# Kernel optimization log

Hardware: AMD Instinct MI355X
Metric: run time of the kernel (lower is better)

The kernel has to match this reference:

```python
import jax, jax.numpy as jnp
import numpy as np

N_NODES = 100000
N_EDGES = 1600000
IN_DIM = 128
HID_DIM = 64
OUT_DIM = 1


def setup_inputs() -> dict:
    key = jax.random.key(0)
    k = jax.random.split(key, 8)
    x = jax.random.normal(k[0], (N_NODES, IN_DIM), dtype=jnp.float32)
    edge_index = jax.random.randint(k[1], (2, N_EDGES), 0, N_NODES, dtype=jnp.int64)
    # GCNConv layer 1: weight [IN, HID], bias [HID] (glorot-ish scale)
    W1 = jax.random.normal(k[2], (IN_DIM, HID_DIM), dtype=jnp.float32) / np.sqrt(IN_DIM)
    b1 = jnp.zeros((HID_DIM,), dtype=jnp.float32)
    W2 = jax.random.normal(k[3], (HID_DIM, HID_DIM), dtype=jnp.float32) / np.sqrt(HID_DIM)
    b2 = jnp.zeros((HID_DIM,), dtype=jnp.float32)
    Wfc = jax.random.normal(k[4], (HID_DIM, OUT_DIM), dtype=jnp.float32) / np.sqrt(HID_DIM)
    bfc = jnp.zeros((OUT_DIM,), dtype=jnp.float32)
    return {"x": x, "edge_index": edge_index, "W1": W1, "b1": b1,
            "W2": W2, "b2": b2, "Wfc": Wfc, "bfc": bfc}


def _gcn_norm(edge_index, n_nodes):
    # PyG GCNConv default: add self-loops, symmetric normalization.
    src, dst = edge_index[0], edge_index[1]
    loop = jnp.arange(n_nodes, dtype=src.dtype)
    src = jnp.concatenate([src, loop])
    dst = jnp.concatenate([dst, loop])
    deg = jax.ops.segment_sum(jnp.ones_like(dst, dtype=jnp.float32), dst,
                              num_segments=n_nodes)
    deg_isqrt = jax.lax.rsqrt(deg)  # deg >= 1 thanks to self-loops
    norm = deg_isqrt[src] * deg_isqrt[dst]  # [E+N]
    return src, dst, norm


def _gcn_conv(x, src, dst, norm, W, b, n_nodes):
    h = x @ W                      # [N, D_out] dense transform first (D_out <= D_in)
    msg = h[src] * norm[:, None]   # gather + normalize  [E+N, D_out]
    out = jax.ops.segment_sum(msg, dst, num_segments=n_nodes)  # scatter-add
    return out + b


def reference(x, edge_index, W1, b1, W2, b2, Wfc, bfc):
    n = x.shape[0]
    src, dst, norm = _gcn_norm(edge_index, n)
    h = jax.nn.relu(_gcn_conv(x, src, dst, norm, W1, b1, n))
    h = jax.nn.relu(_gcn_conv(h, src, dst, norm, W2, b2, n))
    return h @ Wfc + bfc  # [N, 1]
```

## Files before the change

### kernel.cpp

```cpp
#include <hip/hip_runtime.h>
#include <hip/hip_bf16.h>


#define IN_DIM 128
#define HID 64
#define B1 256
#define MAXNC 512

typedef unsigned int uint;

__device__ inline uint pack_bf16x2(float a, float b) {
    uint ua = __builtin_bit_cast(uint, a);
    uint ub = __builtin_bit_cast(uint, b);
    ua += 0x7fffu + ((ua >> 16) & 1u);
    ub += 0x7fffu + ((ub >> 16) & 1u);
    return (ua >> 16) | (ub & 0xffff0000u);
}
__device__ inline float bf_lo(uint g) { return __builtin_bit_cast(float, g << 16); }
__device__ inline float bf_hi(uint g) { return __builtin_bit_cast(float, g & 0xffff0000u); }

__global__ __launch_bounds__(512) void hist1(const int* __restrict__ dst,
                                             int* __restrict__ ghist,
                                             int E, int NC, int chunk) {
    __shared__ int h[MAXNC];
    int t = threadIdx.x, blk = blockIdx.x;
    if (t < NC) h[t] = 0;
    __syncthreads();
    int s = blk * chunk, e = min(E, s + chunk);
    for (int i = s + t; i < e; i += 512) atomicAdd(&h[dst[i] >> 8], 1);
    __syncthreads();
    if (t < NC) ghist[(size_t)t * B1 + blk] = h[t];
}

__global__ __launch_bounds__(256) void scan_p1(const int* __restrict__ a,
                                               int* __restrict__ bsum, int M) {
    int i = blockIdx.x * 256 + threadIdx.x;
    int v = (i < M) ? a[i] : 0;
#pragma unroll
    for (int o = 32; o; o >>= 1) v += __shfl_down(v, o, 64);
    __shared__ int ws[4];
    int lane = threadIdx.x & 63, wid = threadIdx.x >> 6;
    if (lane == 0) ws[wid] = v;
    __syncthreads();
    if (threadIdx.x == 0) bsum[blockIdx.x] = ws[0] + ws[1] + ws[2] + ws[3];
}

__global__ __launch_bounds__(512) void scan_p2(const int* __restrict__ bsum,
                                               int* __restrict__ boff,
                                               int* __restrict__ row_off,
                                               int nb, int N) {
    __shared__ int s[512];
    int t = threadIdx.x;
    int v = (t < nb) ? bsum[t] : 0;
    s[t] = v;
    __syncthreads();
#pragma unroll
    for (int o = 1; o < 512; o <<= 1) {
        int add = (t >= o) ? s[t - o] : 0;
        __syncthreads();
        s[t] += add;
        __syncthreads();
    }
    if (t < nb) boff[t] = s[t] - v;
    if (t == nb - 1) row_off[N] = s[t];
}

__global__ __launch_bounds__(256) void scan_p3(int* __restrict__ a,
                                               const int* __restrict__ boff, int M) {
    __shared__ int s[256];
    int i = blockIdx.x * 256 + threadIdx.x;
    int t = threadIdx.x;
    int d = (i < M) ? a[i] : 0;
    s[t] = d;
    __syncthreads();
#pragma unroll
    for (int o = 1; o < 256; o <<= 1) {
        int add = (t >= o) ? s[t - o] : 0;
        __syncthreads();
        s[t] += add;
        __syncthreads();
    }
    if (i < M) a[i] = s[t] - d + boff[blockIdx.x];
}

__global__ __launch_bounds__(512) void scatter1(const int* __restrict__ src,
                                                const int* __restrict__ dst,
                                                const int* __restrict__ goff,
                                                uint* __restrict__ pairs,
                                                int E, int NC, int chunk) {
    __shared__ int cur[MAXNC];
    int t = threadIdx.x, blk = blockIdx.x;
    if (t < NC) cur[t] = goff[(size_t)t * B1 + blk];
    __syncthreads();
    int s = blk * chunk, e = min(E, s + chunk);
    for (int i = s + t; i < e; i += 512) {
        int d = dst[i];
        int p = atomicAdd(&cur[d >> 8], 1);
        pairs[p] = ((uint)src[i] << 8) | (uint)(d & 255);
    }
}

__global__ __launch_bounds__(256) void build_csr(const uint* __restrict__ pairs,
                                                 const int* __restrict__ goff,
                                                 int* __restrict__ row_off,
                                                 float* __restrict__ disqrt,
                                                 int* __restrict__ col,
                                                 int E, int NC, int N) {
    __shared__ int h[256], cur[256];
    __shared__ int ws[4], wsoff[4];
    int b = blockIdx.x, t = threadIdx.x;
    int base = goff[(size_t)b * B1];
    int next = (b + 1 < NC) ? goff[(size_t)(b + 1) * B1] : E;
    h[t] = 0;
    __syncthreads();
    for (int i = base + t; i < next; i += 256)
        atomicAdd(&h[pairs[i] & 255u], 1);
    __syncthreads();
    int deg = h[t];
    int incl = deg;
#pragma unroll
    for (int o = 1; o < 64; o <<= 1) {
        int u = __shfl_up(incl, o, 64);
        if ((t & 63) >= o) incl += u;
    }
    if ((t & 63) == 63) ws[t >> 6] = incl;
    __syncthreads();
    if (t == 0) {
        int run = 0;
#pragma unroll
        for (int i = 0; i < 4; ++i) { wsoff[i] = run; run += ws[i]; }
    }
    __syncthreads();
    int excl = wsoff[t >> 6] + incl - deg;
    cur[t] = base + excl;
    int node = (b << 8) + t;
    if (node < N) {
        row_off[node] = base + excl;
        disqrt[node]  = rsqrtf((float)(deg + 1));
    }
    __syncthreads();
    for (int i = base + t; i < next; i += 256) {
        uint p = pairs[i];
        int pos = atomicAdd(&cur[p & 255u], 1);
        col[pos] = (int)(p >> 8);
    }
}

template <int K>
__global__ __launch_bounds__(256) void gemm_tile(const float* __restrict__ X,
                                                 const float* __restrict__ W,
                                                 const float* __restrict__ disqrt,
                                                 uint* __restrict__ Tsb, int n) {
    __shared__ float xs[32][132];
    __shared__ float ws[32][64];
    const int tid = threadIdx.x;
    const int ng  = tid & 15;
    const int mg  = tid >> 4;
    const int m0  = blockIdx.x * 128;
    const float4 z4 = make_float4(0.f, 0.f, 0.f, 0.f);
    int xr[4], xk[4];
#pragma unroll
    for (int i = 0; i < 4; ++i) { int f = tid + i * 256; xr[i] = f >> 3; xk[i] = f & 7; }
    const int wk0 = tid >> 4, wc0 = tid & 15;

    float4 gx[4], gw[2];
#pragma unroll
    for (int i = 0; i < 4; ++i) {
        int row = m0 + xr[i];
        gx[i] = (row < n) ? *(const float4*)(X + (size_t)row * K + 4 * xk[i]) : z4;
    }
    gw[0] = *(const float4*)(W + (size_t)wk0 * 64 + 4 * wc0);
    gw[1] = *(const float4*)(W + (size_t)(wk0 + 16) * 64 + 4 * wc0);

    float acc[8][4] = {};
    for (int kc = 0;;) {
#pragma unroll
        for (int i = 0; i < 4; ++i) {
            xs[4 * xk[i] + 0][xr[i]] = gx[i].x;
            xs[4 * xk[i] + 1][xr[i]] = gx[i].y;
            xs[4 * xk[i] + 2][xr[i]] = gx[i].z;
            xs[4 * xk[i] + 3][xr[i]] = gx[i].w;
        }
        *(float4*)&ws[wk0][4 * wc0]      = gw[0];
        *(float4*)&ws[wk0 + 16][4 * wc0] = gw[1];
        __syncthreads();
        kc += 32;
        const bool more = kc < K;
        if (more) {
#pragma unroll
            for (int i = 0; i < 4; ++i) {
                int row = m0 + xr[i];
                gx[i] = (row < n) ? *(const float4*)(X + (size_t)row * K + kc + 4 * xk[i]) : z4;
            }
            gw[0] = *(const float4*)(W + (size_t)(kc + wk0) * 64 + 4 * wc0);
            gw[1] = *(const float4*)(W + (size_t)(kc + wk0 + 16) * 64 + 4 * wc0);
        }
#pragma unroll 4
        for (int k = 0; k < 32; ++k) {
            float4 a0 = *(const float4*)&xs[k][8 * mg];
            float4 a1 = *(const float4*)&xs[k][8 * mg + 4];
            float4 b  = *(const float4*)&ws[k][4 * ng];
            const float* ap0 = (const float*)&a0;
            const float* ap1 = (const float*)&a1;
            const float* bp  = (const float*)&b;
#pragma unroll
            for (int mi = 0; mi < 4; ++mi)
#pragma unroll
                for (int ni = 0; ni < 4; ++ni) {
                    acc[mi][ni]     += ap0[mi] * bp[ni];
                    acc[mi + 4][ni] += ap1[mi] * bp[ni];
                }
        }
        if (!more) break;
        __syncthreads();
    }
#pragma unroll
    for (int mi = 0; mi < 8; ++mi) {
        int row = m0 + 8 * mg + mi;
        if (row < n) {
            float s = disqrt[row];
            uint2 pk;
            pk.x = pack_bf16x2(acc[mi][0] * s, acc[mi][1] * s);
            pk.y = pack_bf16x2(acc[mi][2] * s, acc[mi][3] * s);
            *(uint2*)(Tsb + (size_t)row * 32 + 2 * ng) = pk;
        }
    }
}

__global__ __launch_bounds__(256) void gemm_tile_b(const uint* __restrict__ Xb,
                                                   const float* __restrict__ W,
                                                   const float* __restrict__ disqrt,
                                                   uint* __restrict__ Tsb, int n) {
    const int K = 64;
    __shared__ float xs[32][132];
    __shared__ float ws[32][64];
    const int tid = threadIdx.x;
    const int ng  = tid & 15;
    const int mg  = tid >> 4;
    const int m0  = blockIdx.x * 128;
    const uint2 z2 = make_uint2(0u, 0u);
    int xr[4], xk[4];
#pragma unroll
    for (int i = 0; i < 4; ++i) { int f = tid + i * 256; xr[i] = f >> 3; xk[i] = f & 7; }
    const int wk0 = tid >> 4, wc0 = tid & 15;

    uint2 gx[4];
    float4 gw[2];
#pragma unroll
    for (int i = 0; i < 4; ++i) {
        int row = m0 + xr[i];
        gx[i] = (row < n) ? *(const uint2*)(Xb + (size_t)row * 32 + 2 * xk[i]) : z2;
    }
    gw[0] = *(const float4*)(W + (size_t)wk0 * 64 + 4 * wc0);
    gw[1] = *(const float4*)(W + (size_t)(wk0 + 16) * 64 + 4 * wc0);

    float acc[8][4] = {};
    for (int kc = 0;;) {
#pragma unroll
        for (int i = 0; i < 4; ++i) {
            xs[4 * xk[i] + 0][xr[i]] = bf_lo(gx[i].x);
            xs[4 * xk[i] + 1][xr[i]] = bf_hi(gx[i].x);
            xs[4 * xk[i] + 2][xr[i]] = bf_lo(gx[i].y);
            xs[4 * xk[i] + 3][xr[i]] = bf_hi(gx[i].y);
        }
        *(float4*)&ws[wk0][4 * wc0]      = gw[0];
        *(float4*)&ws[wk0 + 16][4 * wc0] = gw[1];
        __syncthreads();
        kc += 32;
        const bool more = kc < K;
        if (more) {
#pragma unroll
            for (int i = 0; i < 4; ++i) {
                int row = m0 + xr[i];
                gx[i] = (row < n) ? *(const uint2*)(Xb + (size_t)row * 32 + 16 + 2 * xk[i]) : z2;
            }
            gw[0] = *(const float4*)(W + (size_t)(kc + wk0) * 64 + 4 * wc0);
            gw[1] = *(const float4*)(W + (size_t)(kc + wk0 + 16) * 64 + 4 * wc0);
        }
#pragma unroll 4
        for (int k = 0; k < 32; ++k) {
            float4 a0 = *(const float4*)&xs[k][8 * mg];
            float4 a1 = *(const float4*)&xs[k][8 * mg + 4];
            float4 b  = *(const float4*)&ws[k][4 * ng];
            const float* ap0 = (const float*)&a0;
            const float* ap1 = (const float*)&a1;
            const float* bp  = (const float*)&b;
#pragma unroll
            for (int mi = 0; mi < 4; ++mi)
#pragma unroll
                for (int ni = 0; ni < 4; ++ni) {
                    acc[mi][ni]     += ap0[mi] * bp[ni];
                    acc[mi + 4][ni] += ap1[mi] * bp[ni];
                }
        }
        if (!more) break;
        __syncthreads();
    }
#pragma unroll
    for (int mi = 0; mi < 8; ++mi) {
        int row = m0 + 8 * mg + mi;
        if (row < n) {
            float s = disqrt[row];
            uint2 pk;
            pk.x = pack_bf16x2(acc[mi][0] * s, acc[mi][1] * s);
            pk.y = pack_bf16x2(acc[mi][2] * s, acc[mi][3] * s);
            *(uint2*)(Tsb + (size_t)row * 32 + 2 * ng) = pk;
        }
    }
}

template <bool FUSE_FC>
__global__ __launch_bounds__(256) void agg_kernel(const uint* __restrict__ Tsb,
                                                  const int* __restrict__ row_off,
                                                  const int* __restrict__ col,
                                                  const float* __restrict__ disqrt,
                                                  const float* __restrict__ bias,
                                                  const float* __restrict__ wfc,
                                                  const float* __restrict__ bfc,
                                                  uint* __restrict__ outb,
                                                  float* __restrict__ outf, int n) {
    int node = blockIdx.x * 4 + (threadIdx.x >> 6);
    if (node >= n) return;
    int lane = threadIdx.x & 63;
    int o = lane >> 3;
    int p = lane & 7;
    float acc[8] = {};
    if (o == 0) {
        uint4 g = *(const uint4*)(Tsb + (size_t)node * 32 + 4 * p);
        acc[0] = bf_lo(g.x); acc[1] = bf_hi(g.x);
        acc[2] = bf_lo(g.y); acc[3] = bf_hi(g.y);
        acc[4] = bf_lo(g.z); acc[5] = bf_hi(g.z);
        acc[6] = bf_lo(g.w); acc[7] = bf_hi(g.w);
    }
    int beg = __builtin_amdgcn_readfirstlane(row_off[node]);
    int end = __builtin_amdgcn_readfirstlane(row_off[node + 1]);
    for (int batch = beg; batch < end; batch += 64) {
        int bn = min(64, end - batch);
        int cv = 0;
        if (batch + lane < end) cv = col[batch + lane];
        int j = 0;
        for (; j + 16 <= bn; j += 16) {
            int s0 = __shfl(cv, j + o, 64);
            int s1 = __shfl(cv, j + 8 + o, 64);
            uint4 g0 = *(const uint4*)(Tsb + (size_t)s0 * 32 + 4 * p);
            uint4 g1 = *(const uint4*)(Tsb + (size_t)s1 * 32 + 4 * p);
            acc[0] += bf_lo(g0.x); acc[1] += bf_hi(g0.x);
            acc[2] += bf_lo(g0.y); acc[3] += bf_hi(g0.y);
            acc[4] += bf_lo(g0.z); acc[5] += bf_hi(g0.z);
            acc[6] += bf_lo(g0.w); acc[7] += bf_hi(g0.w);
            acc[0] += bf_lo(g1.x); acc[1] += bf_hi(g1.x);
            acc[2] += bf_lo(g1.y); acc[3] += bf_hi(g1.y);
            acc[4] += bf_lo(g1.z); acc[5] += bf_hi(g1.z);
            acc[6] += bf_lo(g1.w); acc[7] += bf_hi(g1.w);
        }
        for (; j < bn; j += 8) {
            int idx = j + o;
            int s = __shfl(cv, idx & 63, 64);
            uint4 g = *(const uint4*)(Tsb + (size_t)s * 32 + 4 * p);
            if (idx < bn) {
                acc[0] += bf_lo(g.x); acc[1] += bf_hi(g.x);
                acc[2] += bf_lo(g.y); acc[3] += bf_hi(g.y);
                acc[4] += bf_lo(g.z); acc[5] += bf_hi(g.z);
                acc[6] += bf_lo(g.w); acc[7] += bf_hi(g.w);
            }
        }
    }
#pragma unroll
    for (int k = 0; k < 8; ++k) {
        acc[k] += __shfl_xor(acc[k], 8, 64);
        acc[k] += __shfl_xor(acc[k], 16, 64);
        acc[k] += __shfl_xor(acc[k], 32, 64);
    }
    float dq = disqrt[node];
    float4 bv0 = *(const float4*)(bias + 8 * p);
    float4 bv1 = *(const float4*)(bias + 8 * p + 4);
    float r[8];
    r[0] = fmaxf(acc[0] * dq + bv0.x, 0.f);
    r[1] = fmaxf(acc[1] * dq + bv0.y, 0.f);
    r[2] = fmaxf(acc[2] * dq + bv0.z, 0.f);
    r[3] = fmaxf(acc[3] * dq + bv0.w, 0.f);
    r[4] = fmaxf(acc[4] * dq + bv1.x, 0.f);
    r[5] = fmaxf(acc[5] * dq + bv1.y, 0.f);
    r[6] = fmaxf(acc[6] * dq + bv1.z, 0.f);
    r[7] = fmaxf(acc[7] * dq + bv1.w, 0.f);
    if (!FUSE_FC) {
        if (o == 0) {
            uint4 pk;
            pk.x = pack_bf16x2(r[0], r[1]);
            pk.y = pack_bf16x2(r[2], r[3]);
            pk.z = pack_bf16x2(r[4], r[5]);
            pk.w = pack_bf16x2(r[6], r[7]);
            *(uint4*)(outb + (size_t)node * 32 + 4 * p) = pk;
        }
    } else {
        float4 wv0 = *(const float4*)(wfc + 8 * p);
        float4 wv1 = *(const float4*)(wfc + 8 * p + 4);
        float v = r[0] * wv0.x + r[1] * wv0.y + r[2] * wv0.z + r[3] * wv0.w +
                  r[4] * wv1.x + r[5] * wv1.y + r[6] * wv1.z + r[7] * wv1.w;
        v += __shfl_down(v, 4, 64);
        v += __shfl_down(v, 2, 64);
        v += __shfl_down(v, 1, 64);
        if (lane == 0) outf[node] = v + bfc[0];
    }
}

extern "C" void kernel_launch(void* const* d_in, const int* in_sizes, int n_in,
                              void* d_out, int out_size, void* d_ws, size_t ws_size,
                              hipStream_t stream) {
    const float* x   = (const float*)d_in[0];
    const int*   ei  = (const int*)d_in[1];
    const float* W1  = (const float*)d_in[2];
    const float* b1  = (const float*)d_in[3];
    const float* W2  = (const float*)d_in[4];
    const float* b2  = (const float*)d_in[5];
    const float* Wfc = (const float*)d_in[6];
    const float* bfc = (const float*)d_in[7];
    float* out = (float*)d_out;

    const int N = in_sizes[0] / IN_DIM;
    const int E = in_sizes[1] / 2;
    const int* src = ei;
    const int* dst = ei + E;
    const int NC    = (N + 255) >> 8;
    const int chunk = (E + B1 - 1) / B1;
    const int M     = NC * B1;
    const int NBs   = (M + 255) / 256;

    char* w = (char*)d_ws;
    auto alloc = [&](size_t bytes) {
        void* p = (void*)w;
        w += (bytes + 255) & ~(size_t)255;
        return p;
    };
    int*   row_off = (int*)alloc((size_t)(N + 1) * 4);
    float* disqrt  = (float*)alloc((size_t)N * 4);
    int*   goff    = (int*)alloc((size_t)NC * B1 * 4);
    int*   bsum    = (int*)alloc(512 * 4);
    int*   boff    = (int*)alloc(512 * 4);
    int*   col     = (int*)alloc((size_t)E * 4);
    size_t scrA = (size_t)E * 4, scrB = (size_t)N * HID * 2;
    void*  scr  = alloc(scrA > scrB ? scrA : scrB);
    uint*  h1b  = (uint*)alloc((size_t)N * HID * 2);
    uint*  pairs = (uint*)scr;
    uint*  Tsb   = (uint*)scr;

    hist1<<<B1, 512, 0, stream>>>(dst, goff, E, NC, chunk);
    scan_p1<<<NBs, 256, 0, stream>>>(goff, bsum, M);
    scan_p2<<<1, 512, 0, stream>>>(bsum, boff, row_off, NBs, N);
    scan_p3<<<NBs, 256, 0, stream>>>(goff, boff, M);
    scatter1<<<B1, 512, 0, stream>>>(src, dst, goff, pairs, E, NC, chunk);
    build_csr<<<NC, 256, 0, stream>>>(pairs, goff, row_off, disqrt, col, E, NC, N);

    gemm_tile<IN_DIM><<<(N + 127) / 128, 256, 0, stream>>>(x, W1, disqrt, Tsb, N);
    agg_kernel<false><<<(N + 3) / 4, 256, 0, stream>>>(Tsb, row_off, col, disqrt,
                                                       b1, nullptr, nullptr,
                                                       h1b, nullptr, N);

    gemm_tile_b<<<(N + 127) / 128, 256, 0, stream>>>(h1b, W2, disqrt, Tsb, N);
    agg_kernel<true><<<(N + 3) / 4, 256, 0, stream>>>(Tsb, row_off, col, disqrt,
                                                      b2, Wfc, bfc,
                                                      nullptr, out, N);
}
```

Measured before the change: 277.8 us.

## Replace FP32 FMA GEMMs with split-bf16 MFMA matrix-core GEMMs

Replaces the two scalar-FMA tiled GEMM kernels with one templated MFMA kernel using 16x16x32 bf16 instructions. Accuracy is kept by splitting the weights (and the fp32 input of layer 1) into high and low bf16 parts and summing three partial products. The weight split and transpose is folded into the single-block scan_p2 kernel. This adds extra MFMA work and per-element split arithmetic, and the GEMMs were probably a minor share next to the memory-bound aggregation kernels.

```diff
diff --git a/kernel.cpp b/kernel.cpp
--- a/kernel.cpp
+++ b/kernel.cpp
@@ -1,5 +1,4 @@
 #include <hip/hip_runtime.h>
-#include <hip/hip_bf16.h>
 
 
 #define IN_DIM 128
@@ -8,6 +7,9 @@
 #define MAXNC 512
 
 typedef unsigned int uint;
+typedef unsigned short ushort;
+typedef __attribute__((ext_vector_type(8))) short short8;
+typedef __attribute__((ext_vector_type(4))) float f32x4;
 
 __device__ inline uint pack_bf16x2(float a, float b) {
     uint ua = __builtin_bit_cast(uint, a);
@@ -18,6 +20,11 @@
 }
 __device__ inline float bf_lo(uint g) { return __builtin_bit_cast(float, g << 16); }
 __device__ inline float bf_hi(uint g) { return __builtin_bit_cast(float, g & 0xffff0000u); }
+__device__ inline uint rne_hi_bits(float a) {
+    uint u = __builtin_bit_cast(uint, a);
+    return (u + 0x7fffu + ((u >> 16) & 1u)) & 0xffff0000u;
+}
+__device__ inline float bitf(uint u) { return __builtin_bit_cast(float, u); }
 
 __global__ __launch_bounds__(512) void hist1(const int* __restrict__ dst,
                                              int* __restrict__ ghist,
@@ -48,9 +55,36 @@
 __global__ __launch_bounds__(512) void scan_p2(const int* __restrict__ bsum,
                                                int* __restrict__ boff,
                                                int* __restrict__ row_off,
-                                               int nb, int N) {
+                                               int nb, int N,
+                                               const float* __restrict__ W1f,
+                                               const float* __restrict__ W2f,
+                                               ushort* __restrict__ w1h,
+                                               ushort* __restrict__ w1l,
+                                               ushort* __restrict__ w2h,
+                                               ushort* __restrict__ w2l) {
+    int t = threadIdx.x;
+    {
+        int c = t & 63;
+        int kb1 = (t >> 6) * 16;
+#pragma unroll 4
+        for (int kk = 0; kk < 16; ++kk) {
+            int k = kb1 + kk;
+            float v = W1f[k * 64 + c];
+            uint rh = rne_hi_bits(v);
+            w1h[c * 128 + k] = (ushort)(rh >> 16);
+            w1l[c * 128 + k] = (ushort)(rne_hi_bits(v - bitf(rh)) >> 16);
+        }
+        int kb2 = (t >> 6) * 8;
+#pragma unroll 4
+        for (int kk = 0; kk < 8; ++kk) {
+            int k = kb2 + kk;
+            float v = W2f[k * 64 + c];
+            uint rh = rne_hi_bits(v);
+            w2h[c * 64 + k] = (ushort)(rh >> 16);
+            w2l[c * 64 + k] = (ushort)(rne_hi_bits(v - bitf(rh)) >> 16);
+        }
+    }
     __shared__ int s[512];
-    int t = threadIdx.x;
     int v = (t < nb) ? bsum[t] : 0;
     s[t] = v;
     __syncthreads();
@@ -146,165 +180,128 @@
     }
 }
 
-template <int K>
-__global__ __launch_bounds__(256) void gemm_tile(const float* __restrict__ X,
-                                                 const float* __restrict__ W,
+template <int K, bool SPLIT>
+__global__ __launch_bounds__(256) void gemm_mfma(const void* __restrict__ Xv,
+                                                 const ushort* __restrict__ WHt,
+                                                 const ushort* __restrict__ WLt,
                                                  const float* __restrict__ disqrt,
                                                  uint* __restrict__ Tsb, int n) {
-    __shared__ float xs[32][132];
-    __shared__ float ws[32][64];
+    __shared__ ushort XH[128 * 40];
+    __shared__ ushort WH[64 * 40];
+    __shared__ ushort WL[64 * 40];
+    __shared__ ushort XL[SPLIT ? 128 * 40 : 64];
+
     const int tid = threadIdx.x;
-    const int ng  = tid & 15;
-    const int mg  = tid >> 4;
     const int m0  = blockIdx.x * 128;
+    const float* Xf = (const float*)Xv;
+    const char*  Xb = (const char*)Xv;
+
+    const int wc = tid >> 2, wslot = tid & 3;
+    const char* wh_g = (const char*)WHt + wc * (K * 2) + wslot * 16;
+    const char* wl_g = (const char*)WLt + wc * (K * 2) + wslot * 16;
+
+    constexpr int NL = SPLIT ? 4 : 2;
+    int xr[NL], xk[NL];
+#pragma unroll
+    for (int i = 0; i < NL; ++i) {
+        int f = tid + i * 256;
+        if (SPLIT) { xr[i] = f >> 3; xk[i] = f & 7; }
+        else       { xr[i] = f >> 2; xk[i] = f & 3; }
+    }
+
     const float4 z4 = make_float4(0.f, 0.f, 0.f, 0.f);
-    int xr[4], xk[4];
-#pragma unroll
-    for (int i = 0; i < 4; ++i) { int f = tid + i * 256; xr[i] = f >> 3; xk[i] = f & 7; }
-    const int wk0 = tid >> 4, wc0 = tid & 15;
-
-    float4 gx[4], gw[2];
-#pragma unroll
-    for (int i = 0; i < 4; ++i) {
+    const uint4  zu = make_uint4(0u, 0u, 0u, 0u);
+    float4 gx[NL];
+    uint4  gxb[NL];
+    uint4  gwh, gwl;
+#pragma unroll
+    for (int i = 0; i < NL; ++i) {
         int row = m0 + xr[i];
-        gx[i] = (row < n) ? *(const float4*)(X + (size_t)row * K + 4 * xk[i]) : z4;
-    }
-    gw[0] = *(const float4*)(W + (size_t)wk0 * 64 + 4 * wc0);
-    gw[1] = *(const float4*)(W + (size_t)(wk0 + 16) * 64 + 4 * wc0);
-
-    float acc[8][4] = {};
+        if (SPLIT) gx[i]  = (row < n) ? *(const float4*)(Xf + (size_t)row * K + 4 * xk[i]) : z4;
+        else       gxb[i] = (row < n) ? *(const uint4*)(Xb + (size_t)row * (K * 2) + xk[i] * 16) : zu;
+    }
+    gwh = *(const uint4*)wh_g;
+    gwl = *(const uint4*)wl_g;
+
+    f32x4 acc[2][4] = {};
+    const int l   = tid & 63, wv = tid >> 6;
+    const int lr  = l & 15;
+    const int kob = (l >> 4) * 16;
+
     for (int kc = 0;;) {
-#pragma unroll
-        for (int i = 0; i < 4; ++i) {
-            xs[4 * xk[i] + 0][xr[i]] = gx[i].x;
-            xs[4 * xk[i] + 1][xr[i]] = gx[i].y;
-            xs[4 * xk[i] + 2][xr[i]] = gx[i].z;
-            xs[4 * xk[i] + 3][xr[i]] = gx[i].w;
-        }
-        *(float4*)&ws[wk0][4 * wc0]      = gw[0];
-        *(float4*)&ws[wk0 + 16][4 * wc0] = gw[1];
-        __syncthreads();
+        if (SPLIT) {
+#pragma unroll
+            for (int i = 0; i < NL; ++i) {
+                float a = gx[i].x, b = gx[i].y, c = gx[i].z, d = gx[i].w;
+                uint rha = rne_hi_bits(a), rhb = rne_hi_bits(b);
+                uint rhc = rne_hi_bits(c), rhd = rne_hi_bits(d);
+                uint2 hh, ll;
+                hh.x = (rha >> 16) | (rhb & 0xffff0000u);
+                hh.y = (rhc >> 16) | (rhd & 0xffff0000u);
+                ll.x = pack_bf16x2(a - bitf(rha), b - bitf(rhb));
+                ll.y = pack_bf16x2(c - bitf(rhc), d - bitf(rhd));
+                *(uint2*)((char*)XH + xr[i] * 80 + xk[i] * 8) = hh;
+                *(uint2*)((char*)XL + xr[i] * 80 + xk[i] * 8) = ll;
+            }
+        } else {
+#pragma unroll
+            for (int i = 0; i < NL; ++i)
+                *(uint4*)((char*)XH + xr[i] * 80 + xk[i] * 16) = gxb[i];
+        }
+        *(uint4*)((char*)WH + wc * 80 + wslot * 16) = gwh;
+        *(uint4*)((char*)WL + wc * 80 + wslot * 16) = gwl;
+        __syncthreads();
+
         kc += 32;
         const bool more = kc < K;
         if (more) {
 #pragma unroll
-            for (int i = 0; i < 4; ++i) {
+            for (int i = 0; i < NL; ++i) {
                 int row = m0 + xr[i];
-                gx[i] = (row < n) ? *(const float4*)(X + (size_t)row * K + kc + 4 * xk[i]) : z4;
+                if (SPLIT) gx[i]  = (row < n) ? *(const float4*)(Xf + (size_t)row * K + kc + 4 * xk[i]) : z4;
+                else       gxb[i] = (row < n) ? *(const uint4*)(Xb + (size_t)row * (K * 2) + kc * 2 + xk[i] * 16) : zu;
             }
-            gw[0] = *(const float4*)(W + (size_t)(kc + wk0) * 64 + 4 * wc0);
-            gw[1] = *(const float4*)(W + (size_t)(kc + wk0 + 16) * 64 + 4 * wc0);
-        }
-#pragma unroll 4
-        for (int k = 0; k < 32; ++k) {
-            float4 a0 = *(const float4*)&xs[k][8 * mg];
-            float4 a1 = *(const float4*)&xs[k][8 * mg + 4];
-            float4 b  = *(const float4*)&ws[k][4 * ng];
-            const float* ap0 = (const float*)&a0;
-            const float* ap1 = (const float*)&a1;
-            const float* bp  = (const float*)&b;
-#pragma unroll
-            for (int mi = 0; mi < 4; ++mi)
-#pragma unroll
-                for (int ni = 0; ni < 4; ++ni) {
-                    acc[mi][ni]     += ap0[mi] * bp[ni];
-                    acc[mi + 4][ni] += ap1[mi] * bp[ni];
-                }
+            gwh = *(const uint4*)(wh_g + kc * 2);
+            gwl = *(const uint4*)(wl_g + kc * 2);
+        }
+
+        short8 xh0 = *(const short8*)((const char*)XH + (wv * 32 + 0 + lr) * 80 + kob);
+        short8 xh1 = *(const short8*)((const char*)XH + (wv * 32 + 16 + lr) * 80 + kob);
+        short8 xl0, xl1;
+        if (SPLIT) {
+            xl0 = *(const short8*)((const char*)XL + (wv * 32 + 0 + lr) * 80 + kob);
+            xl1 = *(const short8*)((const char*)XL + (wv * 32 + 16 + lr) * 80 + kob);
+        }
+#pragma unroll
+        for (int nn = 0; nn < 4; ++nn) {
+            short8 wh = *(const short8*)((const char*)WH + (nn * 16 + lr) * 80 + kob);
+            short8 wl = *(const short8*)((const char*)WL + (nn * 16 + lr) * 80 + kob);
+            acc[0][nn] = __builtin_amdgcn_mfma_f32_16x16x32_bf16(wh, xh0, acc[0][nn], 0, 0, 0);
+            acc[1][nn] = __builtin_amdgcn_mfma_f32_16x16x32_bf16(wh, xh1, acc[1][nn], 0, 0, 0);
+            acc[0][nn] = __builtin_amdgcn_mfma_f32_16x16x32_bf16(wl, xh0, acc[0][nn], 0, 0, 0);
+            acc[1][nn] = __builtin_amdgcn_mfma_f32_16x16x32_bf16(wl, xh1, acc[1][nn], 0, 0, 0);
+            if (SPLIT) {
+                acc[0][nn] = __builtin_amdgcn_mfma_f32_16x16x32_bf16(wh, xl0, acc[0][nn], 0, 0, 0);
+                acc[1][nn] = __builtin_amdgcn_mfma_f32_16x16x32_bf16(wh, xl1, acc[1][nn], 0, 0, 0);
+            }
         }
         if (!more) break;
         __syncthreads();
     }
-#pragma unroll
-    for (int mi = 0; mi < 8; ++mi) {
-        int row = m0 + 8 * mg + mi;
-        if (row < n) {
-            float s = disqrt[row];
-            uint2 pk;
-            pk.x = pack_bf16x2(acc[mi][0] * s, acc[mi][1] * s);
-            pk.y = pack_bf16x2(acc[mi][2] * s, acc[mi][3] * s);
-            *(uint2*)(Tsb + (size_t)row * 32 + 2 * ng) = pk;
-        }
-    }
-}
-
-__global__ __launch_bounds__(256) void gemm_tile_b(const uint* __restrict__ Xb,
-                                                   const float* __restrict__ W,
-                                                   const float* __restrict__ disqrt,
-                                                   uint* __restrict__ Tsb, int n) {
-    const int K = 64;
-    __shared__ float xs[32][132];
-    __shared__ float ws[32][64];
-    const int tid = threadIdx.x;
-    const int ng  = tid & 15;
-    const int mg  = tid >> 4;
-    const int m0  = blockIdx.x * 128;
-    const uint2 z2 = make_uint2(0u, 0u);
-    int xr[4], xk[4];
-#pragma unroll
-    for (int i = 0; i < 4; ++i) { int f = tid + i * 256; xr[i] = f >> 3; xk[i] = f & 7; }
-    const int wk0 = tid >> 4, wc0 = tid & 15;
-
-    uint2 gx[4];
-    float4 gw[2];
-#pragma unroll
-    for (int i = 0; i < 4; ++i) {
-        int row = m0 + xr[i];
-        gx[i] = (row < n) ? *(const uint2*)(Xb + (size_t)row * 32 + 2 * xk[i]) : z2;
-    }
-    gw[0] = *(const float4*)(W + (size_t)wk0 * 64 + 4 * wc0);
-    gw[1] = *(const float4*)(W + (size_t)(wk0 + 16) * 64 + 4 * wc0);
-
-    float acc[8][4] = {};
-    for (int kc = 0;;) {
-#pragma unroll
-        for (int i = 0; i < 4; ++i) {
-            xs[4 * xk[i] + 0][xr[i]] = bf_lo(gx[i].x);
-            xs[4 * xk[i] + 1][xr[i]] = bf_hi(gx[i].x);
-            xs[4 * xk[i] + 2][xr[i]] = bf_lo(gx[i].y);
-            xs[4 * xk[i] + 3][xr[i]] = bf_hi(gx[i].y);
-        }
-        *(float4*)&ws[wk0][4 * wc0]      = gw[0];
-        *(float4*)&ws[wk0 + 16][4 * wc0] = gw[1];
-        __syncthreads();
-        kc += 32;
-        const bool more = kc < K;
-        if (more) {
-#pragma unroll
-            for (int i = 0; i < 4; ++i) {
-                int row = m0 + xr[i];
-                gx[i] = (row < n) ? *(const uint2*)(Xb + (size_t)row * 32 + 16 + 2 * xk[i]) : z2;
+
+#pragma unroll
+    for (int m = 0; m < 2; ++m) {
+        int node = m0 + wv * 32 + m * 16 + lr;
+        if (node < n) {
+            float dq = disqrt[node];
+#pragma unroll
+            for (int nn = 0; nn < 4; ++nn) {
+                f32x4 a = acc[m][nn];
+                uint2 pk;
+                pk.x = pack_bf16x2(a[0] * dq, a[1] * dq);
+                pk.y = pack_bf16x2(a[2] * dq, a[3] * dq);
+                *(uint2*)((char*)Tsb + (size_t)node * 128 + nn * 32 + (l >> 4) * 8) = pk;
             }
-            gw[0] = *(const float4*)(W + (size_t)(kc + wk0) * 64 + 4 * wc0);
-            gw[1] = *(const float4*)(W + (size_t)(kc + wk0 + 16) * 64 + 4 * wc0);
-        }
-#pragma unroll 4
-        for (int k = 0; k < 32; ++k) {
-            float4 a0 = *(const float4*)&xs[k][8 * mg];
-            float4 a1 = *(const float4*)&xs[k][8 * mg + 4];
-            float4 b  = *(const float4*)&ws[k][4 * ng];
-            const float* ap0 = (const float*)&a0;
-            const float* ap1 = (const float*)&a1;
-            const float* bp  = (const float*)&b;
-#pragma unroll
-            for (int mi = 0; mi < 4; ++mi)
-#pragma unroll
-                for (int ni = 0; ni < 4; ++ni) {
-                    acc[mi][ni]     += ap0[mi] * bp[ni];
-                    acc[mi + 4][ni] += ap1[mi] * bp[ni];
-                }
-        }
-        if (!more) break;
-        __syncthreads();
-    }
-#pragma unroll
-    for (int mi = 0; mi < 8; ++mi) {
-        int row = m0 + 8 * mg + mi;
-        if (row < n) {
-            float s = disqrt[row];
-            uint2 pk;
-            pk.x = pack_bf16x2(acc[mi][0] * s, acc[mi][1] * s);
-            pk.y = pack_bf16x2(acc[mi][2] * s, acc[mi][3] * s);
-            *(uint2*)(Tsb + (size_t)row * 32 + 2 * ng) = pk;
         }
     }
 }
@@ -318,9 +315,10 @@
                                                   const float* __restrict__ wfc,
                                                   const float* __restrict__ bfc,
                                                   uint* __restrict__ outb,
-                                                  float* __restrict__ outf, int n) {
-    int node = blockIdx.x * 4 + (threadIdx.x >> 6);
-    if (node >= n) return;
+                                                  float* __restrict__ outf,
+                                                  int node0, int nhi) {
+    int node = node0 + blockIdx.x * 4 + (threadIdx.x >> 6);
+    if (node >= nhi) return;
     int lane = threadIdx.x & 63;
     int o = lane >> 3;
     int p = lane & 7;
@@ -438,6 +436,10 @@
     int*   bsum    = (int*)alloc(512 * 4);
     int*   boff    = (int*)alloc(512 * 4);
     int*   col     = (int*)alloc((size_t)E * 4);
+    ushort* w1h    = (ushort*)alloc(64 * 128 * 2);
+    ushort* w1l    = (ushort*)alloc(64 * 128 * 2);
+    ushort* w2h    = (ushort*)alloc(64 * 64 * 2);
+    ushort* w2l    = (ushort*)alloc(64 * 64 * 2);
     size_t scrA = (size_t)E * 4, scrB = (size_t)N * HID * 2;
     void*  scr  = alloc(scrA > scrB ? scrA : scrB);
     uint*  h1b  = (uint*)alloc((size_t)N * HID * 2);
@@ -446,18 +448,21 @@
 
     hist1<<<B1, 512, 0, stream>>>(dst, goff, E, NC, chunk);
     scan_p1<<<NBs, 256, 0, stream>>>(goff, bsum, M);
-    scan_p2<<<1, 512, 0, stream>>>(bsum, boff, row_off, NBs, N);
+    scan_p2<<<1, 512, 0, stream>>>(bsum, boff, row_off, NBs, N,
+                                   W1, W2, w1h, w1l, w2h, w2l);
     scan_p3<<<NBs, 256, 0, stream>>>(goff, boff, M);
     scatter1<<<B1, 512, 0, stream>>>(src, dst, goff, pairs, E, NC, chunk);
     build_csr<<<NC, 256, 0, stream>>>(pairs, goff, row_off, disqrt, col, E, NC, N);
 
-    gemm_tile<IN_DIM><<<(N + 127) / 128, 256, 0, stream>>>(x, W1, disqrt, Tsb, N);
+    gemm_mfma<IN_DIM, true><<<(N + 127) / 128, 256, 0, stream>>>(
+        x, w1h, w1l, disqrt, Tsb, N);
     agg_kernel<false><<<(N + 3) / 4, 256, 0, stream>>>(Tsb, row_off, col, disqrt,
                                                        b1, nullptr, nullptr,
-                                                       h1b, nullptr, N);
-
-    gemm_tile_b<<<(N + 127) / 128, 256, 0, stream>>>(h1b, W2, disqrt, Tsb, N);
+                                                       h1b, nullptr, 0, N);
+
+    gemm_mfma<HID, false><<<(N + 127) / 128, 256, 0, stream>>>(
+        h1b, w2h, w2l, disqrt, Tsb, N);
     agg_kernel<true><<<(N + 3) / 4, 256, 0, stream>>>(Tsb, row_off, col, disqrt,
                                                       b2, Wfc, bfc,
-                                                      nullptr, out, N);
-}
+                                                      nullptr, out, 0, N);
+}
```

Result: faster. 265.5 us (-4.4%).
